# Performance work log

Hardware: AMD Instinct MI355X
Metric: run time of the kernel (lower is better)

The kernel has to match this reference:

```python
import jax, jax.numpy as jnp
import numpy as np

K = 5          # reassembly kernel size
S = 2          # scale factor
ENC_PAD = 1    # encoder_kernel_size // 2


def _conv2d(x, w, pad):
    return jax.lax.conv_general_dilated(
        x, w, window_strides=(1, 1), padding=[(pad, pad), (pad, pad)],
        dimension_numbers=('NCHW', 'OIHW', 'NCHW'))


def setup_inputs() -> dict:
    key = jax.random.key(0)
    k1, k2, k3 = jax.random.split(key, 3)
    x = jax.random.normal(k1, (2, 256, 40, 40), dtype=jnp.float32)
    # channel compressor: xavier-uniform-ish 1x1 conv weight (64, 256, 1, 1)
    limit = np.sqrt(6.0 / (256 + 64)).astype(np.float32)
    w_comp = jax.random.uniform(k2, (64, 256, 1, 1), dtype=jnp.float32,
                                minval=-limit, maxval=limit)
    # content encoder: normal(0, 0.001), out = k^2*s^2 = 100 channels
    w_enc = 0.001 * jax.random.normal(k3, (100, 64, 3, 3), dtype=jnp.float32)
    return {"x": x, "w_comp": w_comp, "w_enc": w_enc}


def reference(x, w_comp, w_enc):
    b, c, h, w = x.shape
    k2 = K * K
    h_up, w_up = h * S, w * S

    # --- kernel prediction ---
    compressed = _conv2d(x, w_comp, 0)                # (b, 64, h, w)
    kern = _conv2d(compressed, w_enc, ENC_PAD)        # (b, k2*S^2, h, w)
    # pixel shuffle: (b, k2, S, S, h, w) -> (b, k2, h, S, w, S) -> (b, k2, h_up, w_up)
    kern = kern.reshape(b, k2, S, S, h, w).transpose(0, 1, 4, 2, 5, 3)
    kern = kern.reshape(b, k2, h_up * w_up)
    kern = jax.nn.softmax(kern, axis=1)               # softmax over k2

    # --- unfold (im2col, padding K//2) ---
    pad = K // 2
    xp = jnp.pad(x, ((0, 0), (0, 0), (pad, pad), (pad, pad)))
    # (b, c, k2, h, w): channel-major, kernel offsets inner (matches torch F.unfold)
    patches = jnp.stack([xp[:, :, i:i + h, j:j + w]
                         for i in range(K) for j in range(K)], axis=2)
    x_unfold = patches.reshape(b, c, k2, h * w)

    # --- reassembly (faithful to the torch 'efficient' path) ---
    # torch repeat_interleaves x_unfold S^2 times along the h*w axis and
    # multiplies with kernels flattened in (h_up*w_up) row-major order; that
    # pairing is exactly kern reshaped to (b, k2, h*w, S^2):
    kern4 = kern.reshape(b, k2, h * w, S * S)
    out = jnp.einsum('bckp,bkpd->bcpd', x_unfold, kern4)  # (b, c, h*w, S^2)
    return out.reshape(b, c, h_up, w_up)
```

## Files before the change

kernel.cpp:

```cpp
#include <hip/hip_runtime.h>

#define B   2
#define C   256
#define CM  64
#define CE  100
#define H   40
#define W   40
#define HW  1600
#define KK  25

static __device__ __forceinline__ unsigned short f2bf(float f) {
  union { float f; unsigned u; } v; v.f = f;
  unsigned r = v.u + 0x7FFFu + ((v.u >> 16) & 1u);
  return (unsigned short)(r >> 16);
}
static __device__ __forceinline__ float bf2f(unsigned short s) {
  union { float f; unsigned u; } v; v.u = ((unsigned)s) << 16;
  return v.f;
}

__global__ __launch_bounds__(256) void k1_conv1x1(
    const float* __restrict__ x, const float* __restrict__ w,
    unsigned short* __restrict__ pc) {
  const int t = blockIdx.x, ich = blockIdx.y, b = blockIdx.z;
  __shared__ __align__(16) float xs[128 * 64];
  __shared__ __align__(16) float wsA[128 * 64];
  const int tid = threadIdx.x;

  const float4* x4 = (const float4*)(x + ((size_t)b * C + ich * 128) * HW + t * 64);
#pragma unroll
  for (int i = 0; i < 8; i++) {
    int idx = tid + i * 256;
    ((float4*)xs)[idx] = x4[(idx >> 4) * 400 + (idx & 15)];
  }
  const float4* w4 = (const float4*)w;
#pragma unroll
  for (int i = 0; i < 8; i++) {
    int idx = tid + i * 256;
    int icq = idx >> 6, oc = idx & 63;
    float4 f = w4[oc * 64 + ich * 32 + icq];
    wsA[(icq * 4 + 0) * 64 + oc] = f.x;
    wsA[(icq * 4 + 1) * 64 + oc] = f.y;
    wsA[(icq * 4 + 2) * 64 + oc] = f.z;
    wsA[(icq * 4 + 3) * 64 + oc] = f.w;
  }
  __syncthreads();

  const int ty = tid >> 4, tx = tid & 15;
  float acc[4][4];
#pragma unroll
  for (int i = 0; i < 4; i++)
#pragma unroll
    for (int j = 0; j < 4; j++) acc[i][j] = 0.f;

#pragma unroll 4
  for (int icl = 0; icl < 128; icl++) {
    float4 a = *(const float4*)&wsA[icl * 64 + ty * 4];
    float4 bb = *(const float4*)&xs[icl * 64 + tx * 4];
    float av[4] = {a.x, a.y, a.z, a.w};
    float bv[4] = {bb.x, bb.y, bb.z, bb.w};
#pragma unroll
    for (int i = 0; i < 4; i++)
#pragma unroll
      for (int j = 0; j < 4; j++) acc[i][j] += av[i] * bv[j];
  }

  unsigned short* o = pc + (((size_t)ich * B + b) * CM) * HW + t * 64 + tx * 4;
#pragma unroll
  for (int j = 0; j < 4; j++) {
    ushort4 u;
    u.x = f2bf(acc[j][0]); u.y = f2bf(acc[j][1]);
    u.z = f2bf(acc[j][2]); u.w = f2bf(acc[j][3]);
    *(ushort4*)&o[(size_t)(ty * 4 + j) * HW] = u;
  }
}

__global__ __launch_bounds__(256) void k2_conv3x3(
    const unsigned short* __restrict__ pc, const float* __restrict__ w,
    float* __restrict__ enc) {
  const int tile = blockIdx.x, ocq = blockIdx.y, b = blockIdx.z;
  const int ty5 = tile / 5, tx5 = tile % 5;
  __shared__ __align__(16) float cs[CM * 100];
  __shared__ __align__(16) float wsC[4 * 72 * 28];
  float* pacc = wsC;
  const int tid = threadIdx.x;

  const unsigned short* p0 = pc + (size_t)b * CM * HW;
  const unsigned short* p1 = pc + (size_t)(B + b) * CM * HW;
  for (int i = tid; i < CM * 100; i += 256) {
    int ic = i / 100, r = i - ic * 100;
    int yy = r / 10, xx = r - yy * 10;
    int gy = ty5 * 8 + yy - 1, gx = tx5 * 8 + xx - 1;
    float v = 0.f;
    if (gy >= 0 && gy < H && gx >= 0 && gx < W) {
      int idx = ic * HW + gy * W + gx;
      v = bf2f(p0[idx]) + bf2f(p1[idx]);
    }
    cs[i] = v;
  }

  const int wv = tid >> 6, lane = tid & 63, py = lane >> 3, px = lane & 7;
  float acc[KK];
#pragma unroll
  for (int j = 0; j < KK; j++) acc[j] = 0.f;

  const float4* w4 = (const float4*)(w + (size_t)ocq * 25 * 576);
  for (int c = 0; c < 2; c++) {
    if (c) __syncthreads();
    for (int i = tid; i < 1800; i += 256) {
      int ol = i % 25;
      int rr = i / 25;
      int wvs = rr / 18, kq = rr - wvs * 18;
      float4 f = w4[ol * 144 + wvs * 36 + c * 18 + kq];
      float* dst = &wsC[wvs * 2016 + ol];
      int k0 = kq * 4;
      dst[(k0 + 0) * 28] = f.x;
      dst[(k0 + 1) * 28] = f.y;
      dst[(k0 + 2) * 28] = f.z;
      dst[(k0 + 3) * 28] = f.w;
    }
    __syncthreads();

    const float* wslice = &wsC[wv * 2016];
#pragma unroll 1
    for (int icl = 0; icl < 8; icl++) {
      const int ic = wv * 16 + c * 8 + icl;
      const float* csr = &cs[ic * 100 + py * 10 + px];
#pragma unroll
      for (int dy = 0; dy < 3; dy++) {
#pragma unroll
        for (int dx = 0; dx < 3; dx++) {
          float xv = csr[dy * 10 + dx];
          const float4* wr = (const float4*)&wslice[(icl * 9 + dy * 3 + dx) * 28];
          float4 w0 = wr[0], w1 = wr[1], w2 = wr[2], w3 = wr[3];
          float4 w4v = wr[4], w5 = wr[5];
          float w6 = wslice[(icl * 9 + dy * 3 + dx) * 28 + 24];
          acc[0]  += xv * w0.x;  acc[1]  += xv * w0.y;  acc[2]  += xv * w0.z;  acc[3]  += xv * w0.w;
          acc[4]  += xv * w1.x;  acc[5]  += xv * w1.y;  acc[6]  += xv * w1.z;  acc[7]  += xv * w1.w;
          acc[8]  += xv * w2.x;  acc[9]  += xv * w2.y;  acc[10] += xv * w2.z;  acc[11] += xv * w2.w;
          acc[12] += xv * w3.x;  acc[13] += xv * w3.y;  acc[14] += xv * w3.z;  acc[15] += xv * w3.w;
          acc[16] += xv * w4v.x; acc[17] += xv * w4v.y; acc[18] += xv * w4v.z; acc[19] += xv * w4v.w;
          acc[20] += xv * w5.x;  acc[21] += xv * w5.y;  acc[22] += xv * w5.z;  acc[23] += xv * w5.w;
          acc[24] += xv * w6;
        }
      }
    }
  }
  __syncthreads();
#pragma unroll
  for (int j = 0; j < KK; j++) pacc[(wv * KK + j) * 64 + lane] = acc[j];
  __syncthreads();

  float* eb = enc + ((size_t)b * CE + ocq * 25) * HW;
  for (int i = tid; i < 1600; i += 256) {
    int ol = i >> 6, p = i & 63;
    float s = pacc[ol * 64 + p] + pacc[(KK + ol) * 64 + p] +
              pacc[(2 * KK + ol) * 64 + p] + pacc[(3 * KK + ol) * 64 + p];
    int gy = ty5 * 8 + (p >> 3), gx = tx5 * 8 + (p & 7);
    eb[ol * HW + gy * W + gx] = s;
  }
}

__global__ __launch_bounds__(256) void k3_reassemble(
    const float* __restrict__ x, const float* __restrict__ enc,
    float* __restrict__ out) {
  const int i0 = blockIdx.x >> 1;
  const int jh = blockIdx.x & 1;
  const int cq = blockIdx.y;
  const int b = blockIdx.z;

  __shared__ __align__(16) float wlds[20 * KK * 4];
  __shared__ float xsm[64 * 121];

  const int tid = threadIdx.x;

  if (tid < 80) {
    const int e = jh * 80 + tid;
    const int j0 = e >> 2, d = e & 3;
    const int off = ((e >= 80) ? 2 : 0) + (e & 1);
    const int col = ((e >= 80) ? (j0 - 20) : j0) * 2 + (d >> 1);
    const float* ep = enc + (size_t)b * CE * HW + i0 * W + col;
    float v[KK];
    float m = -1e30f;
#pragma unroll
    for (int k = 0; k < KK; k++) {
      v[k] = ep[(k * 4 + off) * HW];
      m = fmaxf(m, v[k]);
    }
    float s = 0.f;
#pragma unroll
    for (int k = 0; k < KK; k++) {
      v[k] = expf(v[k] - m);
      s += v[k];
    }
    const float inv = 1.f / s;
    const int j0l = j0 - jh * 20;
#pragma unroll
    for (int k = 0; k < KK; k++) wlds[(j0l * KK + k) * 4 + d] = v[k] * inv;
  }

  const float* xb = x + ((size_t)b * C + cq * 64) * HW;
  for (int i = tid; i < 64 * 120; i += 256) {
    int c = i / 120;
    int rr = i % 120;
    int r = rr / 24, t = rr % 24;
    int gy = i0 - 2 + r;
    int gx = jh * 20 + t - 2;
    float v = 0.f;
    if (gy >= 0 && gy < H && gx >= 0 && gx < W) v = xb[c * HW + gy * W + gx];
    xsm[c * 121 + r * 24 + t] = v;
  }
  __syncthreads();

  const int wv = tid >> 6;
  const int lane = tid & 63;
  float* ob = out + (((size_t)b * C + cq * 64 + lane) * 6400) + i0 * 160;
  const float* xrow = &xsm[lane * 121];
#pragma unroll 1
  for (int jj = 0; jj < 5; jj++) {
    const int j0l = wv * 5 + jj;
    const int j0 = jh * 20 + j0l;
    float a0 = 0.f, a1 = 0.f, a2 = 0.f, a3 = 0.f;
#pragma unroll
    for (int ki = 0; ki < 5; ki++) {
#pragma unroll
      for (int kj = 0; kj < 5; kj++) {
        float xv = xrow[ki * 24 + j0l + kj];
        float4 w4 = *(const float4*)&wlds[(j0l * KK + ki * 5 + kj) * 4];
        a0 += xv * w4.x;
        a1 += xv * w4.y;
        a2 += xv * w4.z;
        a3 += xv * w4.w;
      }
    }
    float4 o = make_float4(a0, a1, a2, a3);
    *(float4*)&ob[j0 * 4] = o;
  }
}

extern "C" void kernel_launch(void* const* d_in, const int* in_sizes, int n_in,
                              void* d_out, int out_size, void* d_ws, size_t ws_size,
                              hipStream_t stream) {
  const float* x      = (const float*)d_in[0];
  const float* w_comp = (const float*)d_in[1];
  const float* w_enc  = (const float*)d_in[2];
  float* out = (float*)d_out;

  unsigned short* pc = (unsigned short*)d_ws;
  float* enc = (float*)((char*)d_ws + 819200);

  k1_conv1x1<<<dim3(25, 2, B), 256, 0, stream>>>(x, w_comp, pc);
  k2_conv3x3<<<dim3(25, 4, B), 256, 0, stream>>>(pc, w_enc, enc);
  k3_reassemble<<<dim3(80, 4, B), 256, 0, stream>>>(x, enc, out);
}
```

Baseline: 112.7 us.

## Split conv reductions across more blocks with fp32 partials summed downstream

The 1x1 conv now splits input channels into 4 slices instead of 2 and writes fp32 partials instead of bf16. The 3x3 conv grid moves from batch to input-channel quarters, so each block handles both batches and 16 input channels. Each block writes per-quarter partial encoder outputs, and the reassembly kernel sums the four partials before the softmax. This raises block count and parallelism for the small early stages, at the cost of more workspace traffic, extra loads in the reassembly kernel, and higher register pressure from 50 accumulators.

```diff
diff --git a/kernel.cpp b/kernel.cpp
--- a/kernel.cpp
+++ b/kernel.cpp
@@ -9,36 +9,26 @@
 #define HW  1600
 #define KK  25
 
-static __device__ __forceinline__ unsigned short f2bf(float f) {
-  union { float f; unsigned u; } v; v.f = f;
-  unsigned r = v.u + 0x7FFFu + ((v.u >> 16) & 1u);
-  return (unsigned short)(r >> 16);
-}
-static __device__ __forceinline__ float bf2f(unsigned short s) {
-  union { float f; unsigned u; } v; v.u = ((unsigned)s) << 16;
-  return v.f;
-}
-
 __global__ __launch_bounds__(256) void k1_conv1x1(
     const float* __restrict__ x, const float* __restrict__ w,
-    unsigned short* __restrict__ pc) {
+    float* __restrict__ pc) {
   const int t = blockIdx.x, ich = blockIdx.y, b = blockIdx.z;
-  __shared__ __align__(16) float xs[128 * 64];
-  __shared__ __align__(16) float wsA[128 * 64];
+  __shared__ __align__(16) float xs[64 * 64];
+  __shared__ __align__(16) float wsA[64 * 64];
   const int tid = threadIdx.x;
 
-  const float4* x4 = (const float4*)(x + ((size_t)b * C + ich * 128) * HW + t * 64);
-#pragma unroll
-  for (int i = 0; i < 8; i++) {
+  const float4* x4 = (const float4*)(x + ((size_t)b * C + ich * 64) * HW + t * 64);
+#pragma unroll
+  for (int i = 0; i < 4; i++) {
     int idx = tid + i * 256;
     ((float4*)xs)[idx] = x4[(idx >> 4) * 400 + (idx & 15)];
   }
   const float4* w4 = (const float4*)w;
 #pragma unroll
-  for (int i = 0; i < 8; i++) {
+  for (int i = 0; i < 4; i++) {
     int idx = tid + i * 256;
     int icq = idx >> 6, oc = idx & 63;
-    float4 f = w4[oc * 64 + ich * 32 + icq];
+    float4 f = w4[oc * 64 + ich * 16 + icq];
     wsA[(icq * 4 + 0) * 64 + oc] = f.x;
     wsA[(icq * 4 + 1) * 64 + oc] = f.y;
     wsA[(icq * 4 + 2) * 64 + oc] = f.z;
@@ -54,7 +44,7 @@
     for (int j = 0; j < 4; j++) acc[i][j] = 0.f;
 
 #pragma unroll 4
-  for (int icl = 0; icl < 128; icl++) {
+  for (int icl = 0; icl < 64; icl++) {
     float4 a = *(const float4*)&wsA[icl * 64 + ty * 4];
     float4 bb = *(const float4*)&xs[icl * 64 + tx * 4];
     float av[4] = {a.x, a.y, a.z, a.w};
@@ -65,104 +55,114 @@
       for (int j = 0; j < 4; j++) acc[i][j] += av[i] * bv[j];
   }
 
-  unsigned short* o = pc + (((size_t)ich * B + b) * CM) * HW + t * 64 + tx * 4;
-#pragma unroll
-  for (int j = 0; j < 4; j++) {
-    ushort4 u;
-    u.x = f2bf(acc[j][0]); u.y = f2bf(acc[j][1]);
-    u.z = f2bf(acc[j][2]); u.w = f2bf(acc[j][3]);
-    *(ushort4*)&o[(size_t)(ty * 4 + j) * HW] = u;
-  }
+  float* o = pc + ((size_t)ich * B + b) * CM * HW + t * 64 + tx * 4;
+#pragma unroll
+  for (int j = 0; j < 4; j++)
+    *(float4*)&o[(size_t)(ty * 4 + j) * HW] =
+        make_float4(acc[j][0], acc[j][1], acc[j][2], acc[j][3]);
 }
 
 __global__ __launch_bounds__(256) void k2_conv3x3(
-    const unsigned short* __restrict__ pc, const float* __restrict__ w,
-    float* __restrict__ enc) {
-  const int tile = blockIdx.x, ocq = blockIdx.y, b = blockIdx.z;
+    const float* __restrict__ pc, const float* __restrict__ w,
+    float* __restrict__ encP) {
+  const int tile = blockIdx.x, ocq = blockIdx.y, icq = blockIdx.z;
   const int ty5 = tile / 5, tx5 = tile % 5;
-  __shared__ __align__(16) float cs[CM * 100];
-  __shared__ __align__(16) float wsC[4 * 72 * 28];
-  float* pacc = wsC;
+  __shared__ __align__(16) float smem[3200 + 16 * 9 * 28];
+  float* cs  = smem;
+  float* wsb = smem + 3200;
+  float* pacc = smem;
   const int tid = threadIdx.x;
 
-  const unsigned short* p0 = pc + (size_t)b * CM * HW;
-  const unsigned short* p1 = pc + (size_t)(B + b) * CM * HW;
-  for (int i = tid; i < CM * 100; i += 256) {
-    int ic = i / 100, r = i - ic * 100;
-    int yy = r / 10, xx = r - yy * 10;
+  for (int i = tid; i < 3200; i += 256) {
+    int bb = i / 1600, r = i - bb * 1600;
+    int icl = r / 100, rr = r - icl * 100;
+    int yy = rr / 10, xx = rr - yy * 10;
     int gy = ty5 * 8 + yy - 1, gx = tx5 * 8 + xx - 1;
     float v = 0.f;
     if (gy >= 0 && gy < H && gx >= 0 && gx < W) {
-      int idx = ic * HW + gy * W + gx;
-      v = bf2f(p0[idx]) + bf2f(p1[idx]);
+      int o = bb * 102400 + (icq * 16 + icl) * HW + gy * W + gx;
+      v = pc[o] + pc[204800 + o] + pc[409600 + o] + pc[614400 + o];
     }
     cs[i] = v;
   }
+  const float* wb = w + (size_t)(ocq * 25) * 576 + (size_t)(icq * 16) * 9;
+  for (int i = tid; i < 3600; i += 256) {
+    int ol = i / 144, r = i - ol * 144;
+    wsb[r * 28 + ol] = wb[ol * 576 + r];
+  }
+  __syncthreads();
 
   const int wv = tid >> 6, lane = tid & 63, py = lane >> 3, px = lane & 7;
-  float acc[KK];
-#pragma unroll
-  for (int j = 0; j < KK; j++) acc[j] = 0.f;
-
-  const float4* w4 = (const float4*)(w + (size_t)ocq * 25 * 576);
-  for (int c = 0; c < 2; c++) {
-    if (c) __syncthreads();
-    for (int i = tid; i < 1800; i += 256) {
-      int ol = i % 25;
-      int rr = i / 25;
-      int wvs = rr / 18, kq = rr - wvs * 18;
-      float4 f = w4[ol * 144 + wvs * 36 + c * 18 + kq];
-      float* dst = &wsC[wvs * 2016 + ol];
-      int k0 = kq * 4;
-      dst[(k0 + 0) * 28] = f.x;
-      dst[(k0 + 1) * 28] = f.y;
-      dst[(k0 + 2) * 28] = f.z;
-      dst[(k0 + 3) * 28] = f.w;
-    }
-    __syncthreads();
-
-    const float* wslice = &wsC[wv * 2016];
+  float acc[50];
+#pragma unroll
+  for (int j = 0; j < 50; j++) acc[j] = 0.f;
+
 #pragma unroll 1
-    for (int icl = 0; icl < 8; icl++) {
-      const int ic = wv * 16 + c * 8 + icl;
-      const float* csr = &cs[ic * 100 + py * 10 + px];
-#pragma unroll
-      for (int dy = 0; dy < 3; dy++) {
-#pragma unroll
-        for (int dx = 0; dx < 3; dx++) {
-          float xv = csr[dy * 10 + dx];
-          const float4* wr = (const float4*)&wslice[(icl * 9 + dy * 3 + dx) * 28];
-          float4 w0 = wr[0], w1 = wr[1], w2 = wr[2], w3 = wr[3];
-          float4 w4v = wr[4], w5 = wr[5];
-          float w6 = wslice[(icl * 9 + dy * 3 + dx) * 28 + 24];
-          acc[0]  += xv * w0.x;  acc[1]  += xv * w0.y;  acc[2]  += xv * w0.z;  acc[3]  += xv * w0.w;
-          acc[4]  += xv * w1.x;  acc[5]  += xv * w1.y;  acc[6]  += xv * w1.z;  acc[7]  += xv * w1.w;
-          acc[8]  += xv * w2.x;  acc[9]  += xv * w2.y;  acc[10] += xv * w2.z;  acc[11] += xv * w2.w;
-          acc[12] += xv * w3.x;  acc[13] += xv * w3.y;  acc[14] += xv * w3.z;  acc[15] += xv * w3.w;
-          acc[16] += xv * w4v.x; acc[17] += xv * w4v.y; acc[18] += xv * w4v.z; acc[19] += xv * w4v.w;
-          acc[20] += xv * w5.x;  acc[21] += xv * w5.y;  acc[22] += xv * w5.z;  acc[23] += xv * w5.w;
-          acc[24] += xv * w6;
-        }
+  for (int t = 0; t < 4; t++) {
+    const int icl = wv * 4 + t;
+    const float* c0 = &cs[icl * 100 + py * 10 + px];
+    const float* c1 = c0 + 1600;
+    const float* wrow = &wsb[icl * 9 * 28];
+#pragma unroll
+    for (int dy = 0; dy < 3; dy++) {
+#pragma unroll
+      for (int dx = 0; dx < 3; dx++) {
+        float x0 = c0[dy * 10 + dx];
+        float x1 = c1[dy * 10 + dx];
+        const float* wp = &wrow[(dy * 3 + dx) * 28];
+        float4 w0 = *(const float4*)&wp[0],  w1 = *(const float4*)&wp[4];
+        float4 w2 = *(const float4*)&wp[8],  w3 = *(const float4*)&wp[12];
+        float4 w4v = *(const float4*)&wp[16], w5 = *(const float4*)&wp[20];
+        float w6 = wp[24];
+        acc[0]  += x0 * w0.x;  acc[1]  += x0 * w0.y;  acc[2]  += x0 * w0.z;  acc[3]  += x0 * w0.w;
+        acc[4]  += x0 * w1.x;  acc[5]  += x0 * w1.y;  acc[6]  += x0 * w1.z;  acc[7]  += x0 * w1.w;
+        acc[8]  += x0 * w2.x;  acc[9]  += x0 * w2.y;  acc[10] += x0 * w2.z;  acc[11] += x0 * w2.w;
+        acc[12] += x0 * w3.x;  acc[13] += x0 * w3.y;  acc[14] += x0 * w3.z;  acc[15] += x0 * w3.w;
+        acc[16] += x0 * w4v.x; acc[17] += x0 * w4v.y; acc[18] += x0 * w4v.z; acc[19] += x0 * w4v.w;
+        acc[20] += x0 * w5.x;  acc[21] += x0 * w5.y;  acc[22] += x0 * w5.z;  acc[23] += x0 * w5.w;
+        acc[24] += x0 * w6;
+        acc[25] += x1 * w0.x;  acc[26] += x1 * w0.y;  acc[27] += x1 * w0.z;  acc[28] += x1 * w0.w;
+        acc[29] += x1 * w1.x;  acc[30] += x1 * w1.y;  acc[31] += x1 * w1.z;  acc[32] += x1 * w1.w;
+        acc[33] += x1 * w2.x;  acc[34] += x1 * w2.y;  acc[35] += x1 * w2.z;  acc[36] += x1 * w2.w;
+        acc[37] += x1 * w3.x;  acc[38] += x1 * w3.y;  acc[39] += x1 * w3.z;  acc[40] += x1 * w3.w;
+        acc[41] += x1 * w4v.x; acc[42] += x1 * w4v.y; acc[43] += x1 * w4v.z; acc[44] += x1 * w4v.w;
+        acc[45] += x1 * w5.x;  acc[46] += x1 * w5.y;  acc[47] += x1 * w5.z;  acc[48] += x1 * w5.w;
+        acc[49] += x1 * w6;
       }
     }
   }
-  __syncthreads();
-#pragma unroll
-  for (int j = 0; j < KK; j++) pacc[(wv * KK + j) * 64 + lane] = acc[j];
-  __syncthreads();
-
-  float* eb = enc + ((size_t)b * CE + ocq * 25) * HW;
-  for (int i = tid; i < 1600; i += 256) {
-    int ol = i >> 6, p = i & 63;
-    float s = pacc[ol * 64 + p] + pacc[(KK + ol) * 64 + p] +
-              pacc[(2 * KK + ol) * 64 + p] + pacc[(3 * KK + ol) * 64 + p];
-    int gy = ty5 * 8 + (p >> 3), gx = tx5 * 8 + (p & 7);
-    eb[ol * HW + gy * W + gx] = s;
+
+  __syncthreads();
+  if (wv == 1 || wv == 3) {
+    const int slot = wv >> 1;
+#pragma unroll
+    for (int j = 0; j < 50; j++) pacc[slot * 3200 + j * 64 + lane] = acc[j];
+  }
+  __syncthreads();
+  if (wv == 0 || wv == 2) {
+    const int slot = wv >> 1;
+#pragma unroll
+    for (int j = 0; j < 50; j++) acc[j] += pacc[slot * 3200 + j * 64 + lane];
+  }
+  __syncthreads();
+  if (wv == 2) {
+#pragma unroll
+    for (int j = 0; j < 50; j++) pacc[j * 64 + lane] = acc[j];
+  }
+  __syncthreads();
+  if (wv == 0) {
+    const int base_px = (ty5 * 8 + py) * W + tx5 * 8 + px;
+#pragma unroll
+    for (int bb = 0; bb < 2; bb++)
+#pragma unroll
+      for (int ol = 0; ol < 25; ol++)
+        encP[(((size_t)icq * 2 + bb) * CE + ocq * 25 + ol) * HW + base_px] =
+            acc[bb * 25 + ol] + pacc[(bb * 25 + ol) * 64 + lane];
   }
 }
 
 __global__ __launch_bounds__(256) void k3_reassemble(
-    const float* __restrict__ x, const float* __restrict__ enc,
+    const float* __restrict__ x, const float* __restrict__ encP,
     float* __restrict__ out) {
   const int i0 = blockIdx.x >> 1;
   const int jh = blockIdx.x & 1;
@@ -179,12 +179,13 @@
     const int j0 = e >> 2, d = e & 3;
     const int off = ((e >= 80) ? 2 : 0) + (e & 1);
     const int col = ((e >= 80) ? (j0 - 20) : j0) * 2 + (d >> 1);
-    const float* ep = enc + (size_t)b * CE * HW + i0 * W + col;
+    const float* ep = encP + (size_t)b * CE * HW + i0 * W + col;
     float v[KK];
     float m = -1e30f;
 #pragma unroll
     for (int k = 0; k < KK; k++) {
-      v[k] = ep[(k * 4 + off) * HW];
+      int o = (k * 4 + off) * HW;
+      v[k] = ep[o] + ep[320000 + o] + ep[640000 + o] + ep[960000 + o];
       m = fmaxf(m, v[k]);
     }
     float s = 0.f;
@@ -246,10 +247,10 @@
   const float* w_enc  = (const float*)d_in[2];
   float* out = (float*)d_out;
 
-  unsigned short* pc = (unsigned short*)d_ws;
-  float* enc = (float*)((char*)d_ws + 819200);
-
-  k1_conv1x1<<<dim3(25, 2, B), 256, 0, stream>>>(x, w_comp, pc);
-  k2_conv3x3<<<dim3(25, 4, B), 256, 0, stream>>>(pc, w_enc, enc);
-  k3_reassemble<<<dim3(80, 4, B), 256, 0, stream>>>(x, enc, out);
-}
+  float* pc   = (float*)d_ws;
+  float* encP = (float*)((char*)d_ws + 3276800);
+
+  k1_conv1x1<<<dim3(25, 4, B), 256, 0, stream>>>(x, w_comp, pc);
+  k2_conv3x3<<<dim3(25, 4, 4), 256, 0, stream>>>(pc, w_enc, encP);
+  k3_reassemble<<<dim3(80, 4, B), 256, 0, stream>>>(x, encP, out);
+}
```

Measured after the change: 110.3 us. 2.1% less time.
